# Performance work log

Measured on AMD Instinct MI355X. Metric: run time of the kernel, lower is better.

Reference implementation:

```python
import jax, jax.numpy as jnp
import numpy as np

HEADS, K = 8, 7

def setup_inputs() -> dict:
    key = jax.random.key(0)
    ks = jax.random.split(key, 8)
    C = 432
    B, H, W = 1, 56, 56
    n = lambda k, s, std: jax.random.normal(k, s, dtype=jnp.float32) * std
    return {
        "x": n(ks[0], (B, H, W, C), 1.0),
        "qkv_w": n(ks[1], (3 * C, C), 0.02),
        "qkv_b": jnp.zeros((3 * C,), jnp.float32),
        "rpb": n(ks[2], (HEADS, 2 * K - 1, 2 * K - 1), 0.02),
        "conv1_w": n(ks[3], (C, C // 54, K, K), 0.05),   # grouped conv, groups=54 -> 8 in-ch per group
        "conv1_b": jnp.zeros((C,), jnp.float32),
        "conv2_w": n(ks[4], (K * K * HEADS, C, 1, 1), 0.05),
        "conv2_b": jnp.zeros((K * K * HEADS,), jnp.float32),
        "ghost_head": n(ks[5], (C, K, K), 0.02),
        "proj2_w": n(ks[6], (C, 2 * C), 0.02),
        "proj2_b": jnp.zeros((C,), jnp.float32),
    }

def _nat_indices(L, K):
    i = jnp.arange(L)
    ni = jnp.clip(i - K // 2, 0, L - K)                      # clamped window start (NAT semantics)
    idx = ni[:, None] + jnp.arange(K)[None, :]               # [L,K] neighbor coords
    rpb_idx = (K - 1) - (i - ni)[:, None] + jnp.arange(K)[None, :]  # [L,K] rpb lookup
    return idx, rpb_idx

def reference(x, qkv_w, qkv_b, rpb, conv1_w, conv1_b, conv2_w, conv2_b, ghost_head, proj2_w, proj2_b):
    B, H, W, C = x.shape
    hd = C // HEADS
    scale = hd ** -0.5
    qkv = (x @ qkv_w.T + qkv_b).reshape(B, H, W, 3, HEADS, hd)
    qkv = jnp.transpose(qkv, (3, 0, 4, 1, 2, 5))             # [3,B,heads,H,W,hd]
    q, k, v = qkv[0], qkv[1], qkv[2]
    q = q * scale
    idx_i, rpb_i = _nat_indices(H, K)
    idx_j, rpb_j = _nat_indices(W, K)
    ii = idx_i[:, None, :, None]                             # [H,1,K,1]
    jj = idx_j[None, :, None, :]                             # [1,W,1,K]
    # ---- NAT QK + RPB ----
    k_nbr = k[:, :, ii, jj, :]                               # [B,heads,H,W,K,K,hd]
    attn = jnp.einsum('bghwd,bghwuvd->bghwuv', q, k_nbr)
    bias = rpb[:, rpb_i[:, None, :, None], rpb_j[None, :, None, :]]  # [heads,H,W,K,K]
    attn = (attn + bias[None]).reshape(B, HEADS, H, W, K * K)
    attn = jax.nn.softmax(attn, axis=-1)
    # ---- Hadamard conv-attention branch ----
    to_nchw = lambda t: jnp.transpose(t, (0, 2, 3, 1, 4)).reshape(B, H, W, C).transpose(0, 3, 1, 2)
    had = to_nchw(q) * to_nchw(k) * scale                    # note: q already scaled once (faithful)
    h = jax.lax.conv_general_dilated(had, conv1_w, (1, 1), ((K // 2, K // 2), (K // 2, K // 2)),
                                     feature_group_count=54,
                                     dimension_numbers=('NCHW', 'OIHW', 'NCHW')) + conv1_b[None, :, None, None]
    h = jax.nn.gelu(h, approximate=False)
    h = jax.lax.conv_general_dilated(h, conv2_w, (1, 1), ((0, 0), (0, 0)),
                                     dimension_numbers=('NCHW', 'OIHW', 'NCHW')) + conv2_b[None, :, None, None]
    h = jax.nn.softmax(h, axis=1)                            # softmax over all heads*K*K channels
    h_attn = jnp.transpose(h, (0, 2, 3, 1)).reshape(B, H, W, HEADS, K * K).transpose(0, 3, 1, 2, 4)
    attn_A = jnp.concatenate([attn, h_attn], axis=-1)        # [B,heads,H,W,2*K*K]
    # ---- ELSA ghost-head local aggregation (zero-padded centered window, lam=0, gamma=1) ----
    v_tmp = to_nchw(v)                                       # [B,C,H,W]
    a_tmp = jnp.transpose(attn_A, (0, 2, 3, 1, 4)).reshape(B, H, W, -1).transpose(0, 3, 1, 2)
    G = 2 * HEADS                                            # 2*K*K slots per head -> 2*heads attn groups
    a_g = a_tmp.reshape(B, G, K * K, H, W)
    vp = jnp.pad(v_tmp, ((0, 0), (0, 0), (K // 2, K // 2), (K // 2, K // 2)))
    pi = jnp.arange(H)[:, None] + jnp.arange(K)[None, :]     # [H,K]
    pj = jnp.arange(W)[:, None] + jnp.arange(K)[None, :]
    patches = vp[:, :, pi[:, None, :, None], pj[None, :, None, :]].reshape(B, C, H, W, K * K)
    elsa = jnp.einsum('bgchwk,bgkhw->bgchw',
                      patches.reshape(B, G, C // G, H, W, K * K), a_g).reshape(B, C, H, W)
    elsa = elsa + jnp.einsum('bchwk,ck->bchw', patches, ghost_head.reshape(C, K * K))
    attn_tmp = jnp.transpose(elsa, (0, 2, 3, 1)).reshape(B, H, W, HEADS, hd).transpose(0, 3, 1, 2, 4)
    # ---- NAT AV over fused attention (both 49-slot halves share the NAT neighborhood) ----
    a2 = (attn_A[..., :K * K] + attn_A[..., K * K:]).reshape(B, HEADS, H, W, K, K)
    v_nbr = v[:, :, ii, jj, :]                               # [B,heads,H,W,K,K,hd]
    av = jnp.einsum('bghwuv,bghwuvd->bghwd', a2, v_nbr)
    out = jnp.concatenate([av, attn_tmp], axis=-1)           # [B,heads,H,W,2*hd]
    out = jnp.transpose(out, (0, 2, 3, 1, 4)).reshape(B, H, W, 2 * C)
    return out @ proj2_w.T + proj2_b
```

## Files before the change

### kernel.cpp

```cpp
#include <hip/hip_runtime.h>
#include <hip/hip_bf16.h>
#include <math.h>

#define N_PIX 3136
#define NPAD 3200
#define CDIM 432
#define NHEADS 8
#define HD 54
#define KK 49
#define C2 392

typedef __attribute__((ext_vector_type(8))) short bf16x8;
typedef __attribute__((ext_vector_type(4))) float f32x4;
typedef __attribute__((ext_vector_type(8))) unsigned short ushort8;
typedef __attribute__((ext_vector_type(2))) unsigned short ushort2v;

__device__ __forceinline__ void gload_lds16(const void* g, void* l) {
    __builtin_amdgcn_global_load_lds(
        (const __attribute__((address_space(1))) void*)g,
        (__attribute__((address_space(3))) void*)l, 16, 0, 0);
}

__device__ __forceinline__ unsigned short f2bf(float f) {
    __hip_bfloat16 b = __float2bfloat16(f);
    unsigned short u;
    __builtin_memcpy(&u, &b, 2);
    return u;
}

__device__ __forceinline__ size_t perm_off(int r, int k, int Kp) {
    int p = ((k >> 3) & 7) ^ (r & 7);
    return (size_t)r * Kp + ((k >> 6) << 6) + (p << 3) + (k & 7);
}

__device__ __forceinline__ void convert_body(
    const float* __restrict__ src, __hip_bfloat16* __restrict__ dst,
    int Mlog, int Mpad, int Klog, int Kp, int id)
{
    int chunks = Kp >> 3;
    if (id >= Mpad * chunks) return;
    int r = id / chunks, cb = id % chunks;
    int k0 = cb << 3;
    __hip_bfloat16 vv[8];
    #pragma unroll
    for (int e = 0; e < 8; e++) {
        int k = k0 + e;
        float f = (r < Mlog && k < Klog) ? src[(size_t)r * Klog + k] : 0.f;
        vv[e] = __float2bfloat16(f);
    }
    int p = (cb & 7) ^ (r & 7);
    __hip_bfloat16* d = dst + (size_t)r * Kp + ((cb >> 3) << 6) + (p << 3);
    *(ushort8*)d = *(const ushort8*)vv;
}

__global__ __launch_bounds__(256) void prep_kernel(
    const float* __restrict__ x, const float* __restrict__ qkv_w,
    const float* __restrict__ conv2_w, const float* __restrict__ proj2_w,
    const float* __restrict__ ghost,
    __hip_bfloat16* __restrict__ xb, __hip_bfloat16* __restrict__ qkvwb,
    __hip_bfloat16* __restrict__ c2wb, __hip_bfloat16* __restrict__ p2wb,
    float* __restrict__ ghostT, __hip_bfloat16* __restrict__ qkbase)
{
    int b = blockIdx.x;
    if (b < 83) {
        int id = b * 256 + threadIdx.x;
        if (id < CDIM * KK) {
            int cc = id / KK, t = id % KK;
            ghostT[t * CDIM + cc] = ghost[id];
        }
    } else if (b < 769) {
        convert_body(x, xb, 3136, 3136, 432, 448, (b - 83) * 256 + threadIdx.x);
    } else if (b < 1063) {
        convert_body(qkv_w, qkvwb, 1296, 1344, 432, 448, (b - 769) * 256 + threadIdx.x);
    } else if (b < 1161) {
        convert_body(conv2_w, c2wb, 392, 448, 432, 448, (b - 1063) * 256 + threadIdx.x);
    } else if (b < 1357) {
        convert_body(proj2_w, p2wb, 432, 448, 864, 896, (b - 1161) * 256 + threadIdx.x);
    } else {
        int id = (b - 1357) * 256 + threadIdx.x;
        if (id < 2 * 8 * NPAD) {
            __hip_bfloat16* p = qkbase + (size_t)id * 64;
            *(ushort2v*)((unsigned short*)p + 54) = (ushort2v)0;
            *(ushort8*)((unsigned short*)p + 56) = (ushort8)0;
        }
    }
}

__global__ __launch_bounds__(256) void gemm_mfma(
    const __hip_bfloat16* __restrict__ A, const __hip_bfloat16* __restrict__ B,
    const float* __restrict__ bias,
    float* __restrict__ O0, float* __restrict__ O1,
    __hip_bfloat16* __restrict__ VB,
    __hip_bfloat16* __restrict__ QB, __hip_bfloat16* __restrict__ KB,
    int Nlog, int Kp, int mode, float qscale, int ldO)
{
    __shared__ __hip_bfloat16 lA[64 * 64];
    __shared__ __hip_bfloat16 lB[64 * 64];
    const int tid = threadIdx.x;
    const int w = tid >> 6, lane = tid & 63;
    const int row0 = blockIdx.y * 64, col0 = blockIdx.x * 64;
    const int wr = (w >> 1) * 32, wc = (w & 1) * 32;
    const int srow = lane >> 3, schk = lane & 7;
    f32x4 acc[2][2] = {};

    for (int k0 = 0; k0 < Kp; k0 += 64) {
        #pragma unroll
        for (int t = 0; t < 2; t++) {
            int lid = w * 2 + t;
            const __hip_bfloat16* ga =
                A + (size_t)(row0 + lid * 8 + srow) * Kp + k0 + schk * 8;
            gload_lds16(ga, &lA[lid * 8 * 64]);
            const __hip_bfloat16* gb =
                B + (size_t)(col0 + lid * 8 + srow) * Kp + k0 + schk * 8;
            gload_lds16(gb, &lB[lid * 8 * 64]);
        }
        __syncthreads();
        #pragma unroll
        for (int ks = 0; ks < 2; ks++) {
            bf16x8 af[2], bfr[2];
            int c = ks * 4 + (lane >> 4);
            #pragma unroll
            for (int mi = 0; mi < 2; mi++) {
                int ra = wr + mi * 16 + (lane & 15);
                af[mi] = *(const bf16x8*)&lA[ra * 64 + ((c ^ (ra & 7)) << 3)];
                int rb = wc + mi * 16 + (lane & 15);
                bfr[mi] = *(const bf16x8*)&lB[rb * 64 + ((c ^ (rb & 7)) << 3)];
            }
            #pragma unroll
            for (int mi = 0; mi < 2; mi++)
                #pragma unroll
                for (int ni = 0; ni < 2; ni++)
                    acc[mi][ni] = __builtin_amdgcn_mfma_f32_16x16x32_bf16(
                        af[mi], bfr[ni], acc[mi][ni], 0, 0, 0);
        }
        __syncthreads();
    }

    #pragma unroll
    for (int mi = 0; mi < 2; mi++) {
        #pragma unroll
        for (int ni = 0; ni < 2; ni++) {
            #pragma unroll
            for (int rr = 0; rr < 4; rr++) {
                int r = row0 + wr + mi * 16 + (lane >> 4) * 4 + rr;
                int cc = col0 + wc + ni * 16 + (lane & 15);
                if (cc >= Nlog) continue;
                float val = acc[mi][ni][rr] + bias[cc];
                if (mode == 0) {
                    int s = cc / CDIM, cch = cc - s * CDIM;
                    int hh = cch / HD, dd = cch - hh * HD;
                    if (s == 0) {
                        float qv = val * qscale;
                        O0[(size_t)r * CDIM + cch] = qv;
                        QB[((size_t)hh * NPAD + r) * 64 + dd] = __float2bfloat16(qv);
                    } else if (s == 1) {
                        O1[(size_t)r * CDIM + cch] = val;
                        KB[((size_t)hh * NPAD + r) * 64 + dd] = __float2bfloat16(val);
                    } else {
                        VB[((size_t)hh * N_PIX + r) * 64 + dd] = __float2bfloat16(val);
                    }
                } else {
                    O0[(size_t)r * ldO + cc] = val;
                }
            }
        }
    }
}

#define TH 4
__global__ __launch_bounds__(256) void attn_conv1(
    const __hip_bfloat16* __restrict__ qb, const __hip_bfloat16* __restrict__ kb,
    const float* __restrict__ rpb, float* __restrict__ attn,
    const float* __restrict__ q, const float* __restrict__ k,
    const float* __restrict__ w, const float* __restrict__ b,
    __hip_bfloat16* __restrict__ out, float scale)
{
    __shared__ char sraw[26536];
    int tid = threadIdx.x;

    if (blockIdx.x < 448) {
        float (*Sl)[404] = (float(*)[404])sraw;
        float* rpb_l = (float*)(sraw + 16 * 404 * 4);
        int bid = blockIdx.x;
        int nb = (bid & 7) * 56 + (bid >> 3);
        int h = nb / 56, i = nb - (nb / 56) * 56;
        int wv = tid >> 6, lane = tid & 63;
        int l15 = lane & 15, l4 = lane >> 4;
        int ni = min(max(i - 3, 0), 49);

        for (int f = tid; f < 169; f += 256) rpb_l[f] = rpb[h * 169 + f];
        __syncthreads();

        const __hip_bfloat16* qrow = qb + ((size_t)h * NPAD + i * 56) * 64;
        const __hip_bfloat16* kwin = kb + ((size_t)h * NPAD + ni * 56) * 64;

        for (int rt = 0; rt < 4; rt++) {
            bf16x8 af0 = *(const bf16x8*)(qrow + (size_t)(rt * 16 + l15) * 64 + l4 * 8);
            bf16x8 af1 = *(const bf16x8*)(qrow + (size_t)(rt * 16 + l15) * 64 + 32 + l4 * 8);
            for (int ct = wv; ct < 25; ct += 4) {
                bf16x8 b0 = *(const bf16x8*)(kwin + (size_t)(ct * 16 + l15) * 64 + l4 * 8);
                bf16x8 b1 = *(const bf16x8*)(kwin + (size_t)(ct * 16 + l15) * 64 + 32 + l4 * 8);
                f32x4 acc = {};
                acc = __builtin_amdgcn_mfma_f32_16x16x32_bf16(af0, b0, acc, 0, 0, 0);
                acc = __builtin_amdgcn_mfma_f32_16x16x32_bf16(af1, b1, acc, 0, 0, 0);
                int col = ct * 16 + l15;
                #pragma unroll
                for (int r = 0; r < 4; r++)
                    Sl[l4 * 4 + r][col] = acc[r];
            }
            __syncthreads();
            #pragma unroll
            for (int pp = 0; pp < 4; pp++) {
                int j = rt * 16 + wv * 4 + pp;
                if (j < 56) {
                    int n = i * 56 + j;
                    int nj = min(max(j - 3, 0), 49);
                    int t = lane;
                    float logit = -1e30f;
                    if (t < KK) {
                        int u = t / 7, v = t - (t / 7) * 7;
                        int col = u * 56 + nj + v;
                        int ri = 6 - (i - ni) + u;
                        int rj = 6 - (j - nj) + v;
                        logit = Sl[j - rt * 16][col] + rpb_l[ri * 13 + rj];
                    }
                    float m = logit;
                    #pragma unroll
                    for (int off = 32; off; off >>= 1) m = fmaxf(m, __shfl_xor(m, off));
                    float e = (t < KK) ? expf(logit - m) : 0.f;
                    float ssum = e;
                    #pragma unroll
                    for (int off = 32; off; off >>= 1) ssum += __shfl_xor(ssum, off);
                    if (t < KK) attn[(size_t)n * C2 + h * KK + t] = e / ssum;
                }
            }
            __syncthreads();
        }
    } else {
        float (*smem)[8][68] = (float(*)[8][68])sraw;
        int cb = blockIdx.x - 448;
        int g = cb % 54;
        int rt = cb / 54;
        int r0 = rt * TH;
        int waveid = tid >> 6, lane = tid & 63;
        int ic = lane >> 3, oc = lane & 7;

        float* sflat = &smem[0][0][0];
        for (int i = tid; i < 10 * 8 * 68; i += 256) sflat[i] = 0.f;

        float wreg[49];
        {
            const float* wp = w + ((size_t)(g * 8 + oc) * 8 + ic) * 49;
            #pragma unroll
            for (int t = 0; t < 49; t++) wreg[t] = wp[t];
        }
        __syncthreads();

        for (int f = tid; f < 10 * 56 * 2; f += 256) {
            int rr = f / 112, rem = f - rr * 112;
            int pj = rem >> 1, half = rem & 1;
            int pi = r0 - 3 + rr;
            if (pi >= 0 && pi < 56) {
                size_t off = (size_t)(pi * 56 + pj) * CDIM + g * 8 + half * 4;
                float4 qv = *(const float4*)(q + off);
                float4 kv = *(const float4*)(k + off);
                int c0 = half * 4;
                smem[rr][c0 + 0][pj + 3] = qv.x * kv.x * scale;
                smem[rr][c0 + 1][pj + 3] = qv.y * kv.y * scale;
                smem[rr][c0 + 2][pj + 3] = qv.z * kv.z * scale;
                smem[rr][c0 + 3][pj + 3] = qv.w * kv.w * scale;
            }
        }
        __syncthreads();

        int r = r0 + waveid;
        float bias_o = b[g * 8 + oc];
        for (int j0 = 0; j0 < 56; j0 += 4) {
            float acc0 = 0.f, acc1 = 0.f, acc2 = 0.f, acc3 = 0.f;
            #pragma unroll
            for (int u = 0; u < 7; u++) {
                const float* rp = &smem[waveid + u][ic][j0];
                float4 c0 = *(const float4*)(rp);
                float4 c1 = *(const float4*)(rp + 4);
                float4 c2 = *(const float4*)(rp + 8);
                float col[12] = {c0.x, c0.y, c0.z, c0.w,
                                 c1.x, c1.y, c1.z, c1.w,
                                 c2.x, c2.y, c2.z, c2.w};
                #pragma unroll
                for (int v = 0; v < 7; v++) {
                    float wv2 = wreg[u * 7 + v];
                    acc0 += wv2 * col[v + 0];
                    acc1 += wv2 * col[v + 1];
                    acc2 += wv2 * col[v + 2];
                    acc3 += wv2 * col[v + 3];
                }
            }
            float accs[4] = {acc0, acc1, acc2, acc3};
            #pragma unroll
            for (int jj = 0; jj < 4; jj++) {
                float s = accs[jj];
                s += __shfl_xor(s, 8);
                s += __shfl_xor(s, 16);
                s += __shfl_xor(s, 32);
                accs[jj] = s;
            }
            if (ic == 0) {
                #pragma unroll
                for (int jj = 0; jj < 4; jj++) {
                    float a = accs[jj] + bias_o;
                    float gl = 0.5f * a * (1.0f + erff(a * 0.70710678118654752f));
                    int n = r * 56 + j0 + jj;
                    int kch = g * 8 + oc;
                    out[perm_off(n, kch, 448)] = __float2bfloat16(gl);
                }
            }
        }
    }
}

__global__ __launch_bounds__(128) void softmax_pack(
    const float* __restrict__ h2, const float* __restrict__ attn,
    unsigned* __restrict__ pk)
{
    __shared__ float red[128];
    int n = blockIdx.x, tid = threadIdx.x;
    const float* row = h2 + (size_t)n * C2;
    float m = -1e30f;
    float rv[4];
    #pragma unroll
    for (int idx = 0; idx < 4; idx++) {
        int c = tid + idx * 128;
        rv[idx] = (c < C2) ? row[c] : -1e30f;
        m = fmaxf(m, rv[idx]);
    }
    red[tid] = m; __syncthreads();
    for (int s = 64; s; s >>= 1) {
        if (tid < s) red[tid] = fmaxf(red[tid], red[tid + s]);
        __syncthreads();
    }
    m = red[0]; __syncthreads();
    float loc = 0.f;
    #pragma unroll
    for (int idx = 0; idx < 4; idx++) {
        int c = tid + idx * 128;
        if (c < C2) { rv[idx] = expf(rv[idx] - m); loc += rv[idx]; }
    }
    red[tid] = loc; __syncthreads();
    for (int s = 64; s; s >>= 1) {
        if (tid < s) red[tid] += red[tid + s];
        __syncthreads();
    }
    float inv = 1.0f / red[0];
    #pragma unroll
    for (int idx = 0; idx < 4; idx++) {
        int c = tid + idx * 128;
        if (c < C2) {
            float hval = rv[idx] * inv;
            float a = attn[(size_t)n * C2 + c];
            int hh = c / KK, t = c - hh * KK;
            unsigned word = ((unsigned)f2bf(a) << 16) | (unsigned)f2bf(a + hval);
            pk[((size_t)n * 8 + hh) * 52 + t] = word;
        }
    }
}

__global__ __launch_bounds__(256) void combine_fused(
    const __hip_bfloat16* __restrict__ vb, const unsigned* __restrict__ pk,
    const float* __restrict__ ghostT, __hip_bfloat16* __restrict__ comb)
{
    __shared__ float gs[KK * HD];
    int tid = threadIdx.x;
    int lane = tid & 63;

    if (blockIdx.x < 5000) {
        int bid = blockIdx.x;
        int nb = (bid & 7) * 625 + (bid >> 3);
        int h = (nb * 4) / 2500;
        for (int f = tid; f < KK * HD; f += 256) {
            int t = f / HD, dd = f - t * HD;
            gs[f] = ghostT[t * CDIM + h * HD + dd];
        }
        __syncthreads();

        int task = nb * 4 + (tid >> 6);
        task = __builtin_amdgcn_readfirstlane(task);
        int rem = task - h * 2500;
        int i = 3 + rem / 50;
        int j = 3 + (rem - (rem / 50) * 50);
        int n = i * 56 + j;
        int d = (lane < HD) ? lane : (HD - 1);
        bool lo = (d < 27);

        const unsigned* pkrow = pk + ((size_t)n * 8 + h) * 52;
        const __hip_bfloat16* vwin =
            vb + ((size_t)h * N_PIX + (i - 3) * 56 + (j - 3)) * 64 + d;

        float S_ah = 0.f, S_a = 0.f, S_g = 0.f;
        #pragma unroll
        for (int u = 0; u < 7; u++) {
            float vrow[7];
            #pragma unroll
            for (int vv = 0; vv < 7; vv++)
                vrow[vv] = __bfloat162float(vwin[(u * 56 + vv) * 64]);
            #pragma unroll
            for (int vv = 0; vv < 7; vv++) {
                const int t = u * 7 + vv;
                unsigned s = pkrow[t];
                float a  = __uint_as_float(s & 0xFFFF0000u);
                float ah = __uint_as_float(s << 16);
                float gt = gs[t * HD + d];
                S_ah += ah * vrow[vv];
                S_a  += a  * vrow[vv];
                S_g  += gt * vrow[vv];
            }
        }
        if (lane < HD) {
            float av = S_ah;
            float Sh = S_ah - S_a;
            float elsa = S_g + (lo ? S_a : Sh);
            comb[perm_off(n, h * 108 + d, 896)]      = __float2bfloat16(av);
            comb[perm_off(n, h * 108 + 54 + d, 896)] = __float2bfloat16(elsa);
        }
    } else {
        int bid = blockIdx.x - 5000;
        int nb = (bid & 7) * 159 + (bid >> 3);
        int h = (nb * 4) / 636;
        for (int f = tid; f < KK * HD; f += 256) {
            int t = f / HD, dd = f - t * HD;
            gs[f] = ghostT[t * CDIM + h * HD + dd];
        }
        __syncthreads();

        int task = nb * 4 + (tid >> 6);
        task = __builtin_amdgcn_readfirstlane(task);
        int idx = task - h * 636;
        int i, j;
        if (idx < 336) {
            int r = idx / 56;
            i = (r < 3) ? r : 50 + r;
            j = idx - r * 56;
        } else {
            int idx2 = idx - 336;
            i = 3 + idx2 / 6;
            int jj = idx2 - (idx2 / 6) * 6;
            j = (jj < 3) ? jj : 50 + jj;
        }
        int n = i * 56 + j;
        int d = (lane < HD) ? lane : (HD - 1);
        bool lo = (d < 27);

        const unsigned* pkrow = pk + ((size_t)n * 8 + h) * 52;
        int ni = min(max(i - 3, 0), 49), nj = min(max(j - 3, 0), 49);
        const __hip_bfloat16* vhead = vb + (size_t)h * N_PIX * 64 + d;
        const __hip_bfloat16* vbc = vhead + (size_t)(ni * 56 + nj) * 64;

        float S_ahc = 0.f, S_ap = 0.f, S_ahp = 0.f, S_gp = 0.f;
        #pragma unroll
        for (int t = 0; t < KK; t++) {
            const int u = t / 7, vv = t % 7;
            unsigned s = pkrow[t];
            float a  = __uint_as_float(s & 0xFFFF0000u);
            float ah = __uint_as_float(s << 16);
            float vc = __bfloat162float(vbc[(u * 56 + vv) * 64]);
            S_ahc += ah * vc;
            int pi = i + u - 3, pj = j + vv - 3;
            if (pi >= 0 && pi < 56 && pj >= 0 && pj < 56) {
                float vp = __bfloat162float(vhead[(size_t)(pi * 56 + pj) * 64]);
                float gt = gs[t * HD + d];
                S_ahp += ah * vp; S_ap += a * vp; S_gp += gt * vp;
            }
        }
        if (lane < HD) {
            float av = S_ahc;
            float Shp = S_ahp - S_ap;
            float elsa = S_gp + (lo ? S_ap : Shp);
            comb[perm_off(n, h * 108 + d, 896)]      = __float2bfloat16(av);
            comb[perm_off(n, h * 108 + 54 + d, 896)] = __float2bfloat16(elsa);
        }
    }
}

extern "C" void kernel_launch(void* const* d_in, const int* in_sizes, int n_in,
                              void* d_out, int out_size, void* d_ws, size_t ws_size,
                              hipStream_t stream)
{
    const float* x       = (const float*)d_in[0];
    const float* qkv_w   = (const float*)d_in[1];
    const float* qkv_b   = (const float*)d_in[2];
    const float* rpb     = (const float*)d_in[3];
    const float* conv1_w = (const float*)d_in[4];
    const float* conv1_b = (const float*)d_in[5];
    const float* conv2_w = (const float*)d_in[6];
    const float* conv2_b = (const float*)d_in[7];
    const float* ghost   = (const float*)d_in[8];
    const float* proj2_w = (const float*)d_in[9];
    const float* proj2_b = (const float*)d_in[10];
    float* out = (float*)d_out;

    float* ws = (float*)d_ws;
    const size_t NC = (size_t)N_PIX * CDIM;
    const size_t NA = (size_t)N_PIX * C2;
    float* q      = ws;
    float* k      = q + NC;
    float* attn   = k + NC;
    float* hat    = attn + NA;
    float* ghostT = hat + NA;
    unsigned* pk  = (unsigned*)(ghostT + 21168);
    __hip_bfloat16* bfbase = (__hip_bfloat16*)(pk + 1304576);
    __hip_bfloat16* xb     = bfbase;
    __hip_bfloat16* qkvwb  = xb    + (size_t)3136 * 448;
    __hip_bfloat16* c2wb   = qkvwb + (size_t)1344 * 448;
    __hip_bfloat16* p2wb   = c2wb  + (size_t)448 * 448;
    __hip_bfloat16* hb     = p2wb  + (size_t)448 * 896;
    __hip_bfloat16* cb     = hb    + (size_t)3136 * 448;
    __hip_bfloat16* vb16   = cb    + (size_t)3136 * 896;
    __hip_bfloat16* qb16   = vb16  + (size_t)8 * N_PIX * 64;
    __hip_bfloat16* kb16   = qb16  + (size_t)8 * NPAD * 64;

    const float scale = 0.13608276348795434f;

    prep_kernel<<<1557, 256, 0, stream>>>(
        x, qkv_w, conv2_w, proj2_w, ghost, xb, qkvwb, c2wb, p2wb, ghostT, qb16);

    gemm_mfma<<<dim3(21, 49), 256, 0, stream>>>(
        xb, qkvwb, qkv_b, q, k, vb16, qb16, kb16, 1296, 448, 0, scale, 0);

    attn_conv1<<<448 + 756, 256, 0, stream>>>(
        qb16, kb16, rpb, attn, q, k, conv1_w, conv1_b, hb, scale);

    gemm_mfma<<<dim3(7, 49), 256, 0, stream>>>(
        hb, c2wb, conv2_b, hat, nullptr, nullptr, nullptr, nullptr,
        392, 448, 1, 1.f, 392);

    softmax_pack<<<N_PIX, 128, 0, stream>>>(hat, attn, pk);

    combine_fused<<<5000 + 1272, 256, 0, stream>>>(vb16, pk, ghostT, cb);

    gemm_mfma<<<dim3(7, 49), 256, 0, stream>>>(
        cb, p2wb, proj2_b, out, nullptr, nullptr, nullptr, nullptr,
        432, 896, 1, 1.f, 432);
}
```

Measured before the change: 126.1 us.

## Drop fp32 q/k outputs, add bf16 Hadamard pack kernel, taller conv1 tiles

The QKV GEMM no longer writes fp32 q and k copies. A new had_pack kernel computes the scaled q*k Hadamard product from the bf16 q/k buffers into a group-contiguous bf16 layout, which the grouped conv1 branch then reads with one 16-byte load per pixel. The conv branch processes 8 rows per block (two per wave), which halves the number of conv blocks and the halo overhead. GELU now uses a polynomial erf approximation. This adds a kernel launch and an extra bf16 rounding of q*k, and the polynomial may differ slightly from erff.

```diff
diff --git a/kernel.cpp b/kernel.cpp
--- a/kernel.cpp
+++ b/kernel.cpp
@@ -26,6 +26,22 @@
     unsigned short u;
     __builtin_memcpy(&u, &b, 2);
     return u;
+}
+
+__device__ __forceinline__ float bfbits2f(unsigned short u) {
+    return __uint_as_float((unsigned)u << 16);
+}
+
+__device__ __forceinline__ float gelu_exact(float a) {
+    float z = a * 0.70710678118654752f;
+    float s = fabsf(z);
+    float t = 1.0f / (1.0f + 0.3275911f * s);
+    float poly = t * (0.254829592f + t * (-0.284496736f +
+                 t * (1.421413741f + t * (-1.453152027f + t * 1.061405429f))));
+    float e = __expf(-s * s);
+    float er = 1.0f - poly * e;
+    er = (z < 0.f) ? -er : er;
+    return 0.5f * a * (1.0f + er);
 }
 
 __device__ __forceinline__ size_t perm_off(int r, int k, int Kp) {
@@ -89,7 +105,7 @@
 __global__ __launch_bounds__(256) void gemm_mfma(
     const __hip_bfloat16* __restrict__ A, const __hip_bfloat16* __restrict__ B,
     const float* __restrict__ bias,
-    float* __restrict__ O0, float* __restrict__ O1,
+    float* __restrict__ O0,
     __hip_bfloat16* __restrict__ VB,
     __hip_bfloat16* __restrict__ QB, __hip_bfloat16* __restrict__ KB,
     int Nlog, int Kp, int mode, float qscale, int ldO)
@@ -150,14 +166,14 @@
                     int s = cc / CDIM, cch = cc - s * CDIM;
                     int hh = cch / HD, dd = cch - hh * HD;
                     if (s == 0) {
-                        float qv = val * qscale;
-                        O0[(size_t)r * CDIM + cch] = qv;
-                        QB[((size_t)hh * NPAD + r) * 64 + dd] = __float2bfloat16(qv);
+                        QB[((size_t)hh * NPAD + r) * 64 + dd] =
+                            __float2bfloat16(val * qscale);
                     } else if (s == 1) {
-                        O1[(size_t)r * CDIM + cch] = val;
-                        KB[((size_t)hh * NPAD + r) * 64 + dd] = __float2bfloat16(val);
+                        KB[((size_t)hh * NPAD + r) * 64 + dd] =
+                            __float2bfloat16(val);
                     } else {
-                        VB[((size_t)hh * N_PIX + r) * 64 + dd] = __float2bfloat16(val);
+                        VB[((size_t)hh * N_PIX + r) * 64 + dd] =
+                            __float2bfloat16(val);
                     }
                 } else {
                     O0[(size_t)r * ldO + cc] = val;
@@ -167,15 +183,35 @@
     }
 }
 
-#define TH 4
-__global__ __launch_bounds__(256) void attn_conv1(
+__global__ __launch_bounds__(256) void had_pack(
+    const __hip_bfloat16* __restrict__ qb, const __hip_bfloat16* __restrict__ kb,
+    __hip_bfloat16* __restrict__ hadg, float scale)
+{
+    int id = blockIdx.x * 256 + threadIdx.x;
+    if (id >= 54 * N_PIX) return;
+    int g = id / N_PIX;
+    int n = id - g * N_PIX;
+    unsigned short outv[8];
+    #pragma unroll
+    for (int ic = 0; ic < 8; ic++) {
+        int c = g * 8 + ic;
+        int h = c / 54, d = c - h * 54;
+        float qv = __bfloat162float(qb[((size_t)h * NPAD + n) * 64 + d]);
+        float kv = __bfloat162float(kb[((size_t)h * NPAD + n) * 64 + d]);
+        outv[ic] = f2bf(qv * kv * scale);
+    }
+    *(ushort8*)(hadg + (size_t)id * 8) = *(const ushort8*)outv;
+}
+
+#define TH 8
+__global__ __launch_bounds__(256, 2) void attn_conv1(
     const __hip_bfloat16* __restrict__ qb, const __hip_bfloat16* __restrict__ kb,
     const float* __restrict__ rpb, float* __restrict__ attn,
-    const float* __restrict__ q, const float* __restrict__ k,
+    const __hip_bfloat16* __restrict__ hadg,
     const float* __restrict__ w, const float* __restrict__ b,
-    __hip_bfloat16* __restrict__ out, float scale)
-{
-    __shared__ char sraw[26536];
+    __hip_bfloat16* __restrict__ out)
+{
+    __shared__ char sraw[30464];
     int tid = threadIdx.x;
 
     if (blockIdx.x < 448) {
@@ -245,8 +281,9 @@
         int waveid = tid >> 6, lane = tid & 63;
         int ic = lane >> 3, oc = lane & 7;
 
-        float* sflat = &smem[0][0][0];
-        for (int i = tid; i < 10 * 8 * 68; i += 256) sflat[i] = 0.f;
+        float4* sflat4 = (float4*)&smem[0][0][0];
+        for (int i = tid; i < (14 * 8 * 68) / 4; i += 256)
+            sflat4[i] = make_float4(0.f, 0.f, 0.f, 0.f);
 
         float wreg[49];
         {
@@ -256,62 +293,62 @@
         }
         __syncthreads();
 
-        for (int f = tid; f < 10 * 56 * 2; f += 256) {
-            int rr = f / 112, rem = f - rr * 112;
-            int pj = rem >> 1, half = rem & 1;
+        for (int f = tid; f < 14 * 56; f += 256) {
+            int rr = f / 56, pj = f - rr * 56;
             int pi = r0 - 3 + rr;
             if (pi >= 0 && pi < 56) {
-                size_t off = (size_t)(pi * 56 + pj) * CDIM + g * 8 + half * 4;
-                float4 qv = *(const float4*)(q + off);
-                float4 kv = *(const float4*)(k + off);
-                int c0 = half * 4;
-                smem[rr][c0 + 0][pj + 3] = qv.x * kv.x * scale;
-                smem[rr][c0 + 1][pj + 3] = qv.y * kv.y * scale;
-                smem[rr][c0 + 2][pj + 3] = qv.z * kv.z * scale;
-                smem[rr][c0 + 3][pj + 3] = qv.w * kv.w * scale;
-            }
-        }
-        __syncthreads();
-
-        int r = r0 + waveid;
+                ushort8 hv = *(const ushort8*)(hadg +
+                    ((size_t)g * N_PIX + pi * 56 + pj) * 8);
+                #pragma unroll
+                for (int e = 0; e < 8; e++)
+                    smem[rr][e][pj + 3] = bfbits2f(hv[e]);
+            }
+        }
+        __syncthreads();
+
         float bias_o = b[g * 8 + oc];
-        for (int j0 = 0; j0 < 56; j0 += 4) {
-            float acc0 = 0.f, acc1 = 0.f, acc2 = 0.f, acc3 = 0.f;
-            #pragma unroll
-            for (int u = 0; u < 7; u++) {
-                const float* rp = &smem[waveid + u][ic][j0];
-                float4 c0 = *(const float4*)(rp);
-                float4 c1 = *(const float4*)(rp + 4);
-                float4 c2 = *(const float4*)(rp + 8);
-                float col[12] = {c0.x, c0.y, c0.z, c0.w,
-                                 c1.x, c1.y, c1.z, c1.w,
-                                 c2.x, c2.y, c2.z, c2.w};
+        #pragma unroll
+        for (int rr2 = 0; rr2 < 2; rr2++) {
+            int wl = waveid * 2 + rr2;
+            int r = r0 + wl;
+            for (int j0 = 0; j0 < 56; j0 += 4) {
+                float acc0 = 0.f, acc1 = 0.f, acc2 = 0.f, acc3 = 0.f;
                 #pragma unroll
-                for (int v = 0; v < 7; v++) {
-                    float wv2 = wreg[u * 7 + v];
-                    acc0 += wv2 * col[v + 0];
-                    acc1 += wv2 * col[v + 1];
-                    acc2 += wv2 * col[v + 2];
-                    acc3 += wv2 * col[v + 3];
+                for (int u = 0; u < 7; u++) {
+                    const float* rp = &smem[wl + u][ic][j0];
+                    float4 c0 = *(const float4*)(rp);
+                    float4 c1 = *(const float4*)(rp + 4);
+                    float4 c2 = *(const float4*)(rp + 8);
+                    float col[12] = {c0.x, c0.y, c0.z, c0.w,
+                                     c1.x, c1.y, c1.z, c1.w,
+                                     c2.x, c2.y, c2.z, c2.w};
+                    #pragma unroll
+                    for (int v = 0; v < 7; v++) {
+                        float wv2 = wreg[u * 7 + v];
+                        acc0 += wv2 * col[v + 0];
+                        acc1 += wv2 * col[v + 1];
+                        acc2 += wv2 * col[v + 2];
+                        acc3 += wv2 * col[v + 3];
+                    }
                 }
-            }
-            float accs[4] = {acc0, acc1, acc2, acc3};
-            #pragma unroll
-            for (int jj = 0; jj < 4; jj++) {
-                float s = accs[jj];
-                s += __shfl_xor(s, 8);
-                s += __shfl_xor(s, 16);
-                s += __shfl_xor(s, 32);
-                accs[jj] = s;
-            }
-            if (ic == 0) {
+                float accs[4] = {acc0, acc1, acc2, acc3};
                 #pragma unroll
                 for (int jj = 0; jj < 4; jj++) {
-                    float a = accs[jj] + bias_o;
-                    float gl = 0.5f * a * (1.0f + erff(a * 0.70710678118654752f));
-                    int n = r * 56 + j0 + jj;
-                    int kch = g * 8 + oc;
-                    out[perm_off(n, kch, 448)] = __float2bfloat16(gl);
+                    float s = accs[jj];
+                    s += __shfl_xor(s, 8);
+                    s += __shfl_xor(s, 16);
+                    s += __shfl_xor(s, 32);
+                    accs[jj] = s;
+                }
+                if (ic == 0) {
+                    #pragma unroll
+                    for (int jj = 0; jj < 4; jj++) {
+                        float a = accs[jj] + bias_o;
+                        float gl = gelu_exact(a);
+                        int n = r * 56 + j0 + jj;
+                        int kch = g * 8 + oc;
+                        out[perm_off(n, kch, 448)] = __float2bfloat16(gl);
+                    }
                 }
             }
         }
@@ -498,11 +535,8 @@
     float* out = (float*)d_out;
 
     float* ws = (float*)d_ws;
-    const size_t NC = (size_t)N_PIX * CDIM;
     const size_t NA = (size_t)N_PIX * C2;
-    float* q      = ws;
-    float* k      = q + NC;
-    float* attn   = k + NC;
+    float* attn   = ws;
     float* hat    = attn + NA;
     float* ghostT = hat + NA;
     unsigned* pk  = (unsigned*)(ghostT + 21168);
@@ -516,6 +550,7 @@
     __hip_bfloat16* vb16   = cb    + (size_t)3136 * 896;
     __hip_bfloat16* qb16   = vb16  + (size_t)8 * N_PIX * 64;
     __hip_bfloat16* kb16   = qb16  + (size_t)8 * NPAD * 64;
+    __hip_bfloat16* hadg   = kb16  + (size_t)8 * NPAD * 64;
 
     const float scale = 0.13608276348795434f;
 
@@ -523,13 +558,16 @@
         x, qkv_w, conv2_w, proj2_w, ghost, xb, qkvwb, c2wb, p2wb, ghostT, qb16);
 
     gemm_mfma<<<dim3(21, 49), 256, 0, stream>>>(
-        xb, qkvwb, qkv_b, q, k, vb16, qb16, kb16, 1296, 448, 0, scale, 0);
-
-    attn_conv1<<<448 + 756, 256, 0, stream>>>(
-        qb16, kb16, rpb, attn, q, k, conv1_w, conv1_b, hb, scale);
+        xb, qkvwb, qkv_b, nullptr, vb16, qb16, kb16, 1296, 448, 0, scale, 0);
+
+    had_pack<<<(54 * N_PIX + 255) / 256, 256, 0, stream>>>(
+        qb16, kb16, hadg, scale);
+
+    attn_conv1<<<448 + 378, 256, 0, stream>>>(
+        qb16, kb16, rpb, attn, hadg, conv1_w, conv1_b, hb);
 
     gemm_mfma<<<dim3(7, 49), 256, 0, stream>>>(
-        hb, c2wb, conv2_b, hat, nullptr, nullptr, nullptr, nullptr,
+        hb, c2wb, conv2_b, hat, nullptr, nullptr, nullptr,
         392, 448, 1, 1.f, 392);
 
     softmax_pack<<<N_PIX, 128, 0, stream>>>(hat, attn, pk);
@@ -537,6 +575,6 @@
     combine_fused<<<5000 + 1272, 256, 0, stream>>>(vb16, pk, ghostT, cb);
 
     gemm_mfma<<<dim3(7, 49), 256, 0, stream>>>(
-        cb, p2wb, proj2_b, out, nullptr, nullptr, nullptr, nullptr,
+        cb, p2wb, proj2_b, out, nullptr, nullptr, nullptr,
         432, 896, 1, 1.f, 432);
 }
```

New measurement: 166.6 us. +32.1%, slower.
